# Optimization experiments

Hardware: AMD Instinct MI355X
Metric: run time of the kernel (lower is better)

Reference implementation:

```python
import jax, jax.numpy as jnp
import numpy as np
from jax import lax

# ---- fixed configuration (matches init_kwargs / input_specs) ----
L, E, V, F, HU, HL, S = 32, 1024, 2048, 8, 128, 2, 7
D0, D1R, D1E = 512, 129, 640
D = S + 1                      # path dimension = num_slices + 1
SIGLEN = D + D * D + D * D * D # iisignature.siglength(8, 3) = 584
FINAL = F * 2 * SIGLEN         # 9344
EPS = 1e-5                     # BatchNorm eps


def _bn(x, g, b):
    # BatchNorm1d in training mode: biased batch statistics over axis 0
    mu = x.mean(0)
    var = x.var(0)
    return (x - mu) / jnp.sqrt(var + EPS) * g + b


def _mlp(x, Win, bin_, gin, betain, Wh, bh, gh, betah, Wout, bout, gout, betaout):
    # eigf: Linear+BN+ReLU blocks, 1 -> HU -> ... -> HU -> 1
    h = jax.nn.relu(_bn(x @ Win.T + bin_, gin, betain))
    for l in range(HL):
        h = jax.nn.relu(_bn(h @ Wh[l].T + bh[l], gh[l], betah[l]))
    o = jax.nn.relu(_bn(h @ Wout.T + bout, gout, betaout))
    return o[:, 0]


# ---- path signature, level 3, via Chen's identity (replaces iisignature.sig) ----
def _seg(dx):
    s1 = dx
    s2 = jnp.outer(s1, dx).reshape(-1) * 0.5
    s3 = jnp.outer(s2, dx).reshape(-1) / 3.0
    return (s1, s2, s3)


def _chen(Sg, T):
    s1, s2, s3 = Sg
    t1, t2, t3 = T
    r1 = s1 + t1
    r2 = s2 + t2 + jnp.outer(s1, t1).reshape(-1)
    r3 = s3 + t3 + jnp.outer(s1, t2).reshape(-1) + jnp.outer(s2, t1).reshape(-1)
    return (r1, r2, r3)


def _sig3(path):  # path [P, D] -> [SIGLEN]
    dX = path[1:] - path[:-1]

    def step(Sg, dx):
        return _chen(Sg, _seg(dx)), None

    Sg, _ = lax.scan(step, _seg(dX[0]), dX[1:])
    return jnp.concatenate(Sg)


def _diagram_sig(vals, W_proj, b_proj):
    # Conv1d(1, S, kernel=2, stride=2) == pairwise projection; then sort, prepend time axis
    pairs = vals.reshape(-1, 2)                      # [P, 2]
    P = pairs.shape[0]
    proj = jnp.einsum('pk,sk->sp', pairs, W_proj[:, 0, :]) + b_proj[:, None]  # [S, P]
    proj = jnp.sort(proj, axis=-1)
    t = jnp.arange(P, dtype=vals.dtype) / (P * (P + 1) / 2.0)
    path = jnp.concatenate([t[None, :], proj], axis=0).T  # [P, D]
    return _sig3(path)


def setup_inputs() -> dict:
    key = jax.random.key(0)
    ks = iter(jax.random.split(key, 16))
    nrm = lambda kk, shp, sc: jax.random.normal(kk, shp, jnp.float32) * sc
    inp = {
        "eigenvalues": jax.random.uniform(next(ks), (L, E), jnp.float32),
        "eigenvectors_sq": jax.random.uniform(next(ks), (L, E, V), jnp.float32) / E,
        "dgm0": jax.random.randint(next(ks), (L, F, D0), 0, V, jnp.int32),
        "dgm1rel": jax.random.randint(next(ks), (L, F, D1R), 0, V, jnp.int32),
        "dgm1ext": jax.random.randint(next(ks), (L, F, D1E), 0, V, jnp.int32),
        "mlp_Win": nrm(next(ks), (F, HU, 1), 1.0),
        "mlp_bin": jnp.zeros((F, HU), jnp.float32),
        "mlp_gin": jnp.ones((F, HU), jnp.float32),
        "mlp_betain": jnp.zeros((F, HU), jnp.float32),
        "mlp_Wh": nrm(next(ks), (F, HL, HU, HU), 1.0 / np.sqrt(HU)),
        "mlp_bh": jnp.zeros((F, HL, HU), jnp.float32),
        "mlp_gh": jnp.ones((F, HL, HU), jnp.float32),
        "mlp_betah": jnp.zeros((F, HL, HU), jnp.float32),
        "mlp_Wout": nrm(next(ks), (F, 1, HU), 1.0 / np.sqrt(HU)),
        "mlp_bout": jnp.zeros((F, 1), jnp.float32),
        "mlp_gout": jnp.ones((F, 1), jnp.float32),
        "mlp_betaout": jnp.zeros((F, 1), jnp.float32),
        "W_proj": nrm(next(ks), (S, 1, 2), 0.7),
        "b_proj": jnp.zeros((S,), jnp.float32),
        "W_fin": nrm(next(ks), (1, FINAL), 1.0 / np.sqrt(FINAL)),
        "b_fin": jnp.zeros((1,), jnp.float32),
        "g_fin": jnp.ones((1,), jnp.float32),
        "beta_fin": jnp.zeros((1,), jnp.float32),
    }
    return inp


def reference(eigenvalues, eigenvectors_sq, dgm0, dgm1rel, dgm1ext,
              mlp_Win, mlp_bin, mlp_gin, mlp_betain,
              mlp_Wh, mlp_bh, mlp_gh, mlp_betah,
              mlp_Wout, mlp_bout, mlp_gout, mlp_betaout,
              W_proj, b_proj, W_fin, b_fin, g_fin, beta_fin):
    flat = eigenvalues.reshape(-1, 1)  # [L*E, 1], sample-major like the torch flatten
    evs = jax.vmap(lambda *p: _mlp(flat, *p))(
        mlp_Win, mlp_bin, mlp_gin, mlp_betain,
        mlp_Wh, mlp_bh, mlp_gh, mlp_betah,
        mlp_Wout, mlp_bout, mlp_gout, mlp_betaout)  # [F, L*E]
    # per-sample filtration values: evs_transformed[:, slice_i] @ eigvecsq_i
    f = jnp.einsum('fle,lev->lfv', evs.reshape(F, L, E), eigenvectors_sq)  # [L, F, V]
    fv = f.reshape(L * F, V)
    d0 = jnp.take_along_axis(fv, dgm0.reshape(L * F, D0), axis=1)
    rel = jnp.take_along_axis(fv, dgm1rel.reshape(L * F, D1R), axis=1)
    # torch.arange(len-1, 0, -1): reversed, dropping element 0
    Dgm0 = jnp.concatenate([d0, rel[:, 1:][:, ::-1]], axis=1)  # [L*F, 640]
    Dgm1 = jnp.take_along_axis(fv, dgm1ext.reshape(L * F, D1E), axis=1)
    sig0 = jax.vmap(lambda v: _diagram_sig(v, W_proj, b_proj))(Dgm0)  # [L*F, SIGLEN]
    sig1 = jax.vmap(lambda v: _diagram_sig(v, W_proj, b_proj))(Dgm1)
    x = jnp.concatenate([sig0, sig1], axis=-1).reshape(L, FINAL)
    out = x @ W_fin.T + b_fin  # dropout p=0.0 -> identity
    return _bn(out, g_fin, beta_fin)  # [L, 1]
```

## Files before the change

### kernel.cpp

```cpp
#include <hip/hip_runtime.h>
#include <cfloat>
#include <math.h>

#define N_SAMP 32768
#define FF 8
#define HU 128
#define EE 1024
#define VV 2048
#define PP 320
#define SIGLEN 584
#define FINAL_W 9344

typedef unsigned short u16;
typedef unsigned int u32;
typedef short s16x8 __attribute__((ext_vector_type(8)));
typedef float f32x4 __attribute__((ext_vector_type(4)));

__device__ __forceinline__ u16 f2bf(float v) {
  u32 u = __float_as_uint(v);
  return (u16)((u + 0x7fffu + ((u >> 16) & 1u)) >> 16);
}
__device__ __forceinline__ float bf2f(u16 h) {
  return __uint_as_float(((u32)h) << 16);
}
__device__ __forceinline__ void split3(float v, u16& h, u16& m, u16& l) {
  h = f2bf(v);
  float r = v - bf2f(h);
  m = f2bf(r);
  float r2 = r - bf2f(m);
  l = f2bf(r2);
}

__device__ __forceinline__ double wave_red(double v) {
#pragma unroll
  for (int off = 32; off > 0; off >>= 1) v += __shfl_xor(v, off, 64);
  return v;
}

__global__ __launch_bounds__(256) void k_wsplit(const float* __restrict__ W,
                                                u16* __restrict__ Hh, u16* __restrict__ Hm,
                                                u16* __restrict__ Hl, int n) {
  int i = blockIdx.x * 256 + threadIdx.x;
  if (i >= n) return;
  u16 h, m, l;
  split3(W[i], h, m, l);
  Hh[i] = h; Hm[i] = m; Hl[i] = l;
}

__global__ __launch_bounds__(256) void k_xstats(const float* __restrict__ x,
                                                double* __restrict__ xst) {
  const int tid = threadIdx.x;
  double s1 = 0.0, s2 = 0.0;
  for (int i = tid; i < N_SAMP; i += 256) { double v = (double)x[i]; s1 += v; s2 += v * v; }
  __shared__ double r1[4], r2[4];
  double w1 = wave_red(s1), w2 = wave_red(s2);
  int wave = tid >> 6, lane = tid & 63;
  if (lane == 0) { r1[wave] = w1; r2[wave] = w2; }
  __syncthreads();
  if (tid == 0) {
    xst[0] = r1[0] + r1[1] + r1[2] + r1[3];
    xst[1] = r2[0] + r2[1] + r2[2] + r2[3];
  }
}

template<int MODE>
__global__ __launch_bounds__(256, 2)
void k_mgemm(const float* __restrict__ Ain,
             const double* __restrict__ xstats,
             const float* __restrict__ w_in,
             const float* __restrict__ g_in,
             const float* __restrict__ beta_in,
             const float* __restrict__ sc,
             const float* __restrict__ sh,
             const u16* __restrict__ Wh_,
             const u16* __restrict__ Wm_,
             const u16* __restrict__ Wl_,
             const float* __restrict__ bb, int bstride,
             float* __restrict__ Yt_out,
             double* __restrict__ stats) {
  __shared__ u16 SB[6][128 * 40];
  __shared__ float p0[HU], p1[HU], biasl[HU], xl[HU];
  u16* Ah = SB[0]; u16* Am = SB[1]; u16* Al = SB[2];
  u16* Bh = SB[3]; u16* Bm = SB[4]; u16* Bl = SB[5];

  const int tid = threadIdx.x;
  const int f = blockIdx.y;
  const int m0 = blockIdx.x * 128;
  const int lane = tid & 63, ln = tid & 15, quad = (tid >> 4) & 3, wave = tid >> 6;

  if (tid < HU) {
    biasl[tid] = bb[(size_t)f * bstride + tid];
    if (MODE == 0) {
      double mx = xstats[0] * (1.0 / 32768.0);
      double vx = xstats[1] * (1.0 / 32768.0) - mx * mx;
      if (vx < 0) vx = 0;
      float w = w_in[f * HU + tid];
      double inv = 1.0 / sqrt((double)w * (double)w * vx + 1e-5);
      float sj = (float)inv * g_in[f * HU + tid] * w;
      p0[tid] = sj;
      p1[tid] = beta_in[f * HU + tid] - (float)mx * sj;
      xl[tid] = Ain[m0 + tid];
    } else {
      p0[tid] = sc[f * HU + tid];
      p1[tid] = sh[f * HU + tid];
    }
  }

  f32x4 acc[2][8];
#pragma unroll
  for (int mt = 0; mt < 2; ++mt)
#pragma unroll
    for (int u = 0; u < 8; ++u) acc[mt][u] = (f32x4){0.f, 0.f, 0.f, 0.f};

  __syncthreads();

  for (int kk = 0; kk < 128; kk += 32) {
    if (MODE == 0) {
      const int m = tid >> 1, kh = (tid & 1) * 16;
      const float xv = xl[m];
      u32 ph[8], pm[8], pl[8];
#pragma unroll
      for (int jp = 0; jp < 8; ++jp) {
        u16 h0, m_0, l0, h1, m_1, l1;
        int k = kh + jp * 2;
        split3(fmaxf(fmaf(xv, p0[kk + k], p1[kk + k]), 0.f), h0, m_0, l0);
        split3(fmaxf(fmaf(xv, p0[kk + k + 1], p1[kk + k + 1]), 0.f), h1, m_1, l1);
        ph[jp] = (u32)h0 | ((u32)h1 << 16);
        pm[jp] = (u32)m_0 | ((u32)m_1 << 16);
        pl[jp] = (u32)l0 | ((u32)l1 << 16);
      }
      int off = m * 40 + kh;
      *(uint4*)&Ah[off] = make_uint4(ph[0], ph[1], ph[2], ph[3]);
      *(uint4*)&Ah[off + 8] = make_uint4(ph[4], ph[5], ph[6], ph[7]);
      *(uint4*)&Am[off] = make_uint4(pm[0], pm[1], pm[2], pm[3]);
      *(uint4*)&Am[off + 8] = make_uint4(pm[4], pm[5], pm[6], pm[7]);
      *(uint4*)&Al[off] = make_uint4(pl[0], pl[1], pl[2], pl[3]);
      *(uint4*)&Al[off + 8] = make_uint4(pl[4], pl[5], pl[6], pl[7]);
    } else {
#pragma unroll
      for (int r = 0; r < 4; ++r) {
        int flat = tid + r * 256;
        int m = flat & 127, kq = flat >> 7;
        const float* src = Ain + ((size_t)(f * HU + kk + kq * 4)) * N_SAMP + m0 + m;
        u32 ph[2], pm[2], pl[2];
#pragma unroll
        for (int ip = 0; ip < 2; ++ip) {
          int k = kq * 4 + ip * 2;
          float v0 = fmaxf(fmaf(src[(size_t)(ip * 2) * N_SAMP], p0[kk + k], p1[kk + k]), 0.f);
          float v1 = fmaxf(fmaf(src[(size_t)(ip * 2 + 1) * N_SAMP], p0[kk + k + 1], p1[kk + k + 1]), 0.f);
          u16 h0, m_0, l0, h1, m_1, l1;
          split3(v0, h0, m_0, l0);
          split3(v1, h1, m_1, l1);
          ph[ip] = (u32)h0 | ((u32)h1 << 16);
          pm[ip] = (u32)m_0 | ((u32)m_1 << 16);
          pl[ip] = (u32)l0 | ((u32)l1 << 16);
        }
        int off = m * 40 + kq * 4;
        *(uint2*)&Ah[off] = make_uint2(ph[0], ph[1]);
        *(uint2*)&Am[off] = make_uint2(pm[0], pm[1]);
        *(uint2*)&Al[off] = make_uint2(pl[0], pl[1]);
      }
    }
#pragma unroll
    for (int r = 0; r < 2; ++r) {
      int flat = tid + r * 256;
      int n = flat >> 2, c = flat & 3;
      size_t g = (size_t)f * (2 * HU * HU) + (size_t)n * HU + kk + c * 8;
      int off = n * 40 + c * 8;
      *(uint4*)&Bh[off] = *(const uint4*)&Wh_[g];
      *(uint4*)&Bm[off] = *(const uint4*)&Wm_[g];
      *(uint4*)&Bl[off] = *(const uint4*)&Wl_[g];
    }
    __syncthreads();
    s16x8 af0[3], af1[3];
    {
      int r0 = (wave * 32 + ln) * 40 + quad * 8;
      int r1 = (wave * 32 + 16 + ln) * 40 + quad * 8;
      af0[0] = *(const s16x8*)&Ah[r0]; af0[1] = *(const s16x8*)&Am[r0]; af0[2] = *(const s16x8*)&Al[r0];
      af1[0] = *(const s16x8*)&Ah[r1]; af1[1] = *(const s16x8*)&Am[r1]; af1[2] = *(const s16x8*)&Al[r1];
    }
#pragma unroll
    for (int u = 0; u < 8; ++u) {
      int bo = (u * 16 + ln) * 40 + quad * 8;
      s16x8 bh = *(const s16x8*)&Bh[bo];
      s16x8 bm = *(const s16x8*)&Bm[bo];
      s16x8 bl = *(const s16x8*)&Bl[bo];
      f32x4 a0 = acc[0][u], a1 = acc[1][u];
      a0 = __builtin_amdgcn_mfma_f32_16x16x32_bf16(af0[0], bh, a0, 0, 0, 0);
      a1 = __builtin_amdgcn_mfma_f32_16x16x32_bf16(af1[0], bh, a1, 0, 0, 0);
      a0 = __builtin_amdgcn_mfma_f32_16x16x32_bf16(af0[1], bh, a0, 0, 0, 0);
      a1 = __builtin_amdgcn_mfma_f32_16x16x32_bf16(af1[1], bh, a1, 0, 0, 0);
      a0 = __builtin_amdgcn_mfma_f32_16x16x32_bf16(af0[0], bm, a0, 0, 0, 0);
      a1 = __builtin_amdgcn_mfma_f32_16x16x32_bf16(af1[0], bm, a1, 0, 0, 0);
      a0 = __builtin_amdgcn_mfma_f32_16x16x32_bf16(af0[2], bh, a0, 0, 0, 0);
      a1 = __builtin_amdgcn_mfma_f32_16x16x32_bf16(af1[2], bh, a1, 0, 0, 0);
      a0 = __builtin_amdgcn_mfma_f32_16x16x32_bf16(af0[1], bm, a0, 0, 0, 0);
      a1 = __builtin_amdgcn_mfma_f32_16x16x32_bf16(af1[1], bm, a1, 0, 0, 0);
      a0 = __builtin_amdgcn_mfma_f32_16x16x32_bf16(af0[0], bl, a0, 0, 0, 0);
      a1 = __builtin_amdgcn_mfma_f32_16x16x32_bf16(af1[0], bl, a1, 0, 0, 0);
      acc[0][u] = a0; acc[1][u] = a1;
    }
    __syncthreads();
  }

  float cs1[8], cs2[8];
#pragma unroll
  for (int u = 0; u < 8; ++u) { cs1[u] = 0.f; cs2[u] = 0.f; }
#pragma unroll
  for (int u = 0; u < 8; ++u) {
    float b = biasl[u * 16 + ln];
#pragma unroll
    for (int mt = 0; mt < 2; ++mt) {
#pragma unroll
      for (int reg = 0; reg < 4; ++reg) {
        float v = acc[mt][u][reg] + b;
        acc[mt][u][reg] = v;
        cs1[u] += v;
        cs2[u] = fmaf(v, v, cs2[u]);
      }
      float4 st = make_float4(acc[mt][u][0], acc[mt][u][1], acc[mt][u][2], acc[mt][u][3]);
      *(float4*)&Yt_out[((size_t)(f * HU + u * 16 + ln)) * N_SAMP + m0 + wave * 32 + mt * 16 + quad * 4] = st;
    }
  }
  float* red1 = (float*)&SB[0][0];
  float* red2 = red1 + 2048;
  int wq = wave * 4 + quad;
#pragma unroll
  for (int u = 0; u < 8; ++u) {
    red1[wq * 128 + u * 16 + ln] = cs1[u];
    red2[wq * 128 + u * 16 + ln] = cs2[u];
  }
  __syncthreads();
  {
    int which = tid >> 7, n = tid & 127;
    const float* rp = which ? red2 : red1;
    float s = 0.f;
#pragma unroll
    for (int r = 0; r < 16; ++r) s += rp[r * 128 + n];
    atomicAdd(&stats[(f * HU + n) * 2 + which], (double)s);
  }
}

__global__ __launch_bounds__(256) void k_fin(const double* __restrict__ stats,
                                             const float* __restrict__ g,
                                             const float* __restrict__ beta,
                                             int per_f, int gstride, int count,
                                             float* __restrict__ sc, float* __restrict__ sh) {
  int idx = blockIdx.x * 256 + threadIdx.x;
  if (idx >= count) return;
  int f = idx / per_f, j = idx - f * per_f;
  double S1 = stats[idx * 2 + 0], S2 = stats[idx * 2 + 1];
  double mean = S1 * (1.0 / 32768.0);
  double var = S2 * (1.0 / 32768.0) - mean * mean;
  if (var < 0) var = 0;
  double inv = 1.0 / sqrt(var + 1e-5);
  float gg = g[f * gstride + j];
  float scv = (float)inv * gg;
  sc[idx] = scv;
  sh[idx] = beta[f * gstride + j] - (float)mean * scv;
}

__global__ __launch_bounds__(256, 4) void k_outlayer(const float* __restrict__ Yt,
                                                     const float* __restrict__ sc2,
                                                     const float* __restrict__ sh2,
                                                     const float* __restrict__ Wout,
                                                     const float* __restrict__ bout,
                                                     float* __restrict__ evs_pre,
                                                     double* __restrict__ stats3) {
  __shared__ float wj[HU], scl[HU], shl[HU];
  const int tid = threadIdx.x;
  const int f = blockIdx.y;
  const int i = blockIdx.x * 256 + tid;
  if (tid < HU) {
    wj[tid] = Wout[f * HU + tid];
    scl[tid] = sc2[f * HU + tid];
    shl[tid] = sh2[f * HU + tid];
  }
  __syncthreads();
  const float* base = Yt + (size_t)f * HU * N_SAMP + i;
  float acc = 0.f;
#pragma unroll
  for (int j = 0; j < HU; ++j) {
    float y = base[(size_t)j * N_SAMP];
    acc = fmaf(fmaxf(fmaf(y, scl[j], shl[j]), 0.f), wj[j], acc);
  }
  float yo = acc + bout[f];
  evs_pre[(size_t)f * N_SAMP + i] = yo;
  double v = (double)yo;
  double s1 = wave_red(v), s2 = wave_red(v * v);
  __shared__ double r1[4], r2[4];
  int wave = tid >> 6, lane = tid & 63;
  if (lane == 0) { r1[wave] = s1; r2[wave] = s2; }
  __syncthreads();
  if (tid == 0) atomicAdd(&stats3[f * 2 + 0], r1[0] + r1[1] + r1[2] + r1[3]);
  if (tid == 1) atomicAdd(&stats3[f * 2 + 1], r2[0] + r2[1] + r2[2] + r2[3]);
}

__global__ __launch_bounds__(256) void k_einsum(const float* __restrict__ evs_pre,
                                                const float* __restrict__ sc3,
                                                const float* __restrict__ sh3,
                                                const float* __restrict__ eig,
                                                float* __restrict__ fv) {
  __shared__ float ev[FF * EE];
  const int tid = threadIdx.x;
  const int l = blockIdx.y;
  const int v0 = blockIdx.x * 256;
#pragma unroll
  for (int r = 0; r < 32; ++r) {
    int q = tid + r * 256;
    int f = q >> 10, e = q & 1023;
    float y = evs_pre[(size_t)f * N_SAMP + l * EE + e];
    ev[q] = fmaxf(fmaf(y, sc3[f], sh3[f]), 0.f);
  }
  __syncthreads();
  const float* up = eig + (size_t)l * EE * VV + v0 + tid;
  float acc[8] = {0, 0, 0, 0, 0, 0, 0, 0};
  for (int e0 = 0; e0 < EE; e0 += 32) {
    float u[32];
#pragma unroll
    for (int t = 0; t < 32; ++t) u[t] = up[(size_t)(e0 + t) * VV];
#pragma unroll
    for (int t = 0; t < 32; ++t) {
#pragma unroll
      for (int f = 0; f < 8; ++f) acc[f] = fmaf(ev[f * EE + e0 + t], u[t], acc[f]);
    }
  }
#pragma unroll
  for (int f = 0; f < 8; ++f) fv[((size_t)(l * FF + f)) * VV + v0 + tid] = acc[f];
}

__global__ __launch_bounds__(256) void k_diagram(const float* __restrict__ fv,
                                                 const int* __restrict__ dgm0,
                                                 const int* __restrict__ dgm1rel,
                                                 const int* __restrict__ dgm1ext,
                                                 const float* __restrict__ Wp,
                                                 const float* __restrict__ bp,
                                                 float* __restrict__ xbuf) {
  __shared__ float vals[640];
  __shared__ float ps[7 * 512];
  __shared__ float dXl[320][8];
  const int tid = threadIdx.x;
  const int bid = blockIdx.x;
  const int row = bid >> 1;
  const int c = bid & 1;
  const float* fvr = fv + (size_t)row * VV;

  for (int k = tid; k < 640; k += 256) {
    int idx;
    if (c == 0) idx = (k < 512) ? dgm0[(size_t)row * 512 + k] : dgm1rel[(size_t)row * 129 + (640 - k)];
    else        idx = dgm1ext[(size_t)row * 640 + k];
    vals[k] = fvr[idx];
  }
  __syncthreads();
  for (int q = tid; q < 7 * 512; q += 256) {
    int s = q >> 9, p = q & 511;
    float pv = 3.402823466e+38f;
    if (p < PP) pv = fmaf(Wp[2 * s + 1], vals[2 * p + 1], fmaf(Wp[2 * s], vals[2 * p], bp[s]));
    ps[s * 512 + p] = pv;
  }
  for (int k = 2; k <= 512; k <<= 1) {
    for (int j = k >> 1; j > 0; j >>= 1) {
      __syncthreads();
      for (int q = tid; q < 1792; q += 256) {
        int s = q >> 8, ip = q & 255;
        int i = ((ip & ~(j - 1)) << 1) | (ip & (j - 1));
        int p2 = i | j;
        float a = ps[s * 512 + i], b = ps[s * 512 + p2];
        bool up = ((i & k) == 0);
        if ((a > b) == up) { ps[s * 512 + i] = b; ps[s * 512 + p2] = a; }
      }
    }
  }
  __syncthreads();
  for (int q = tid; q < 319 * 8; q += 256) {
    int p = q >> 3, d = q & 7;
    dXl[p][d] = (d == 0) ? (1.0f / 51360.0f)
                         : ps[(d - 1) * 512 + p + 1] - ps[(d - 1) * 512 + p];
  }
  __syncthreads();
  if (tid < 64) {
    const int a = tid >> 3, b = tid & 7;
    float s1a = 0.f, s2r = 0.f;
    float s3r[8] = {0, 0, 0, 0, 0, 0, 0, 0};
    for (int p = 0; p < 319; ++p) {
      float4 dlo = *(const float4*)&dXl[p][0];
      float4 dhi = *(const float4*)&dXl[p][4];
      float dxa = dXl[p][a];
      float dxb = dXl[p][b];
      float coefA = fmaf(dxa, (1.f / 3.f), s1a);
      float w = fmaf(0.5f * dxb, coefA, s2r);
      s2r = fmaf(dxb, fmaf(0.5f, dxa, s1a), s2r);
      s3r[0] = fmaf(w, dlo.x, s3r[0]);
      s3r[1] = fmaf(w, dlo.y, s3r[1]);
      s3r[2] = fmaf(w, dlo.z, s3r[2]);
      s3r[3] = fmaf(w, dlo.w, s3r[3]);
      s3r[4] = fmaf(w, dhi.x, s3r[4]);
      s3r[5] = fmaf(w, dhi.y, s3r[5]);
      s3r[6] = fmaf(w, dhi.z, s3r[6]);
      s3r[7] = fmaf(w, dhi.w, s3r[7]);
      s1a += dxa;
    }
    const int l = row >> 3, ff = row & 7;
    float* xr = xbuf + (size_t)l * FINAL_W + ff * (2 * SIGLEN) + c * SIGLEN;
    if ((tid & 7) == 0) xr[a] = s1a;
    xr[8 + tid] = s2r;
    float* s3p = xr + 72 + tid * 8;
    *(float4*)(s3p + 0) = make_float4(s3r[0], s3r[1], s3r[2], s3r[3]);
    *(float4*)(s3p + 4) = make_float4(s3r[4], s3r[5], s3r[6], s3r[7]);
  }
}

__global__ __launch_bounds__(256) void k_rowdot(const float* __restrict__ xbuf,
                                                const float* __restrict__ Wf,
                                                const float* __restrict__ bf,
                                                double* __restrict__ outpre) {
  const int tid = threadIdx.x, l = blockIdx.x;
  const float* xr = xbuf + (size_t)l * FINAL_W;
  double acc = 0.0;
  for (int k = tid; k < FINAL_W; k += 256) acc += (double)xr[k] * (double)Wf[k];
  acc = wave_red(acc);
  __shared__ double r[4];
  int wave = tid >> 6, lane = tid & 63;
  if (lane == 0) r[wave] = acc;
  __syncthreads();
  if (tid == 0) outpre[l] = r[0] + r[1] + r[2] + r[3] + (double)bf[0];
}

__global__ __launch_bounds__(64) void k_bnfin(const double* __restrict__ outpre,
                                              const float* __restrict__ g,
                                              const float* __restrict__ beta,
                                              float* __restrict__ dout) {
  int i = threadIdx.x;
  double v = (i < 32) ? outpre[i] : 0.0;
  double s1 = wave_red(v);
  double s2 = wave_red(v * v);
  double mean = s1 * (1.0 / 32.0);
  double var = s2 * (1.0 / 32.0) - mean * mean;
  if (var < 0) var = 0;
  double inv = 1.0 / sqrt(var + 1e-5);
  if (i < 32) dout[i] = (float)((v - mean) * inv * (double)g[0] + (double)beta[0]);
}

extern "C" void kernel_launch(void* const* d_in, const int* in_sizes, int n_in,
                              void* d_out, int out_size, void* d_ws, size_t ws_size,
                              hipStream_t stream) {
  const float* eig     = (const float*)d_in[0];
  const float* eigsq   = (const float*)d_in[1];
  const int*   dgm0    = (const int*)d_in[2];
  const int*   dgm1rel = (const int*)d_in[3];
  const int*   dgm1ext = (const int*)d_in[4];
  const float* Win     = (const float*)d_in[5];
  const float* gin     = (const float*)d_in[7];
  const float* betain  = (const float*)d_in[8];
  const float* Wh      = (const float*)d_in[9];
  const float* bh      = (const float*)d_in[10];
  const float* gh      = (const float*)d_in[11];
  const float* betah   = (const float*)d_in[12];
  const float* Wout    = (const float*)d_in[13];
  const float* bout    = (const float*)d_in[14];
  const float* gout    = (const float*)d_in[15];
  const float* betaout = (const float*)d_in[16];
  const float* Wp      = (const float*)d_in[17];
  const float* bp      = (const float*)d_in[18];
  const float* Wfin    = (const float*)d_in[19];
  const float* bfin    = (const float*)d_in[20];
  const float* gfin    = (const float*)d_in[21];
  const float* betafin = (const float*)d_in[22];

  char* ws = (char*)d_ws;
  float*  Yt      = (float*)(ws);
  float*  evs_pre = (float*)(ws + 134217728u);
  float*  fv      = (float*)(ws + 135266304u);
  float*  xbuf    = (float*)(ws + 137363456u);
  float*  sc1     = (float*)(ws + 138559488u);
  float*  sh1     = sc1 + 1024;
  float*  sc2     = sc1 + 2048;
  float*  sh2     = sc1 + 3072;
  float*  sc3     = sc1 + 4096;
  float*  sh3     = sc1 + 4160;
  double* stats1  = (double*)(ws + 138576384u);
  double* stats2  = stats1 + 2048;
  double* stats3  = stats1 + 4096;
  double* xstats  = stats1 + 4112;
  double* outpre  = stats1 + 4114;
  u16*    Whh     = (u16*)(ws + 138612736u);
  u16*    Whm     = (u16*)(ws + 139137024u);
  u16*    Whl     = (u16*)(ws + 139661312u);

  hipMemsetAsync(stats1, 0, 4114 * sizeof(double), stream);

  k_wsplit<<<1024, 256, 0, stream>>>(Wh, Whh, Whm, Whl, FF * 2 * HU * HU);
  k_xstats<<<1, 256, 0, stream>>>(eig, xstats);
  k_mgemm<0><<<dim3(256, FF), 256, 0, stream>>>(eig, xstats, Win, gin, betain,
                                                nullptr, nullptr,
                                                Whh, Whm, Whl,
                                                bh, 256, Yt, stats1);
  k_fin<<<4, 256, 0, stream>>>(stats1, gh, betah, 128, 256, 1024, sc1, sh1);
  k_mgemm<1><<<dim3(256, FF), 256, 0, stream>>>(Yt, nullptr, nullptr, nullptr, nullptr,
                                                sc1, sh1,
                                                Whh + HU * HU, Whm + HU * HU, Whl + HU * HU,
                                                bh + 128, 256, Yt, stats2);
  k_fin<<<4, 256, 0, stream>>>(stats2, gh + 128, betah + 128, 128, 256, 1024, sc2, sh2);
  k_outlayer<<<dim3(128, FF), 256, 0, stream>>>(Yt, sc2, sh2, Wout, bout, evs_pre, stats3);
  k_fin<<<1, 256, 0, stream>>>(stats3, gout, betaout, 1, 1, 8, sc3, sh3);
  k_einsum<<<dim3(8, 32), 256, 0, stream>>>(evs_pre, sc3, sh3, eigsq, fv);
  k_diagram<<<512, 256, 0, stream>>>(fv, dgm0, dgm1rel, dgm1ext, Wp, bp, xbuf);
  k_rowdot<<<32, 256, 0, stream>>>(xbuf, Wfin, bfin, outpre);
  k_bnfin<<<1, 64, 0, stream>>>(outpre, gfin, betafin, (float*)d_out);
}
```

Baseline: 743.8 us.

## Fuse BN finalize into consumers, switch MLP activations to row-major, drop LDS staging

The separate weight-split and input-stats kernels are merged into one prep kernel, and the stats reduction now uses atomics across blocks. The three BN-finalize kernels are removed; each consumer recomputes scale and shift from the raw double stats. The hidden activation buffer changes from feature-major to sample-major, so the MLP GEMM loads A fragments directly from global memory into registers and reads B fragments straight from global instead of staging both in LDS with barriers. This cuts launches and syncs, but output stores become strided scalar writes, and B fragments are re-read from global/L2 by every wave.

```diff
diff --git a/kernel.cpp b/kernel.cpp
--- a/kernel.cpp
+++ b/kernel.cpp
@@ -37,29 +37,28 @@
   return v;
 }
 
-__global__ __launch_bounds__(256) void k_wsplit(const float* __restrict__ W,
-                                                u16* __restrict__ Hh, u16* __restrict__ Hm,
-                                                u16* __restrict__ Hl, int n) {
-  int i = blockIdx.x * 256 + threadIdx.x;
-  if (i >= n) return;
-  u16 h, m, l;
-  split3(W[i], h, m, l);
-  Hh[i] = h; Hm[i] = m; Hl[i] = l;
-}
-
-__global__ __launch_bounds__(256) void k_xstats(const float* __restrict__ x,
-                                                double* __restrict__ xst) {
-  const int tid = threadIdx.x;
-  double s1 = 0.0, s2 = 0.0;
-  for (int i = tid; i < N_SAMP; i += 256) { double v = (double)x[i]; s1 += v; s2 += v * v; }
-  __shared__ double r1[4], r2[4];
-  double w1 = wave_red(s1), w2 = wave_red(s2);
-  int wave = tid >> 6, lane = tid & 63;
-  if (lane == 0) { r1[wave] = w1; r2[wave] = w2; }
-  __syncthreads();
-  if (tid == 0) {
-    xst[0] = r1[0] + r1[1] + r1[2] + r1[3];
-    xst[1] = r2[0] + r2[1] + r2[2] + r2[3];
+__global__ __launch_bounds__(256) void k_prep(const float* __restrict__ W,
+                                              u16* __restrict__ Hh, u16* __restrict__ Hm,
+                                              u16* __restrict__ Hl,
+                                              const float* __restrict__ x,
+                                              double* __restrict__ xst) {
+  const int b = blockIdx.x, tid = threadIdx.x;
+  if (b < 1024) {
+    int i = b * 256 + tid;
+    u16 h, m, l;
+    split3(W[i], h, m, l);
+    Hh[i] = h; Hm[i] = m; Hl[i] = l;
+  } else {
+    int i0 = (b - 1024) * 512 + tid;
+    double v0 = (double)x[i0], v1 = (double)x[i0 + 256];
+    double s1 = wave_red(v0 + v1);
+    double s2 = wave_red(v0 * v0 + v1 * v1);
+    __shared__ double r1[4], r2[4];
+    int wave = tid >> 6, lane = tid & 63;
+    if (lane == 0) { r1[wave] = s1; r2[wave] = s2; }
+    __syncthreads();
+    if (tid == 0) atomicAdd(&xst[0], r1[0] + r1[1] + r1[2] + r1[3]);
+    if (tid == 1) atomicAdd(&xst[1], r2[0] + r2[1] + r2[2] + r2[3]);
   }
 }
 
@@ -70,23 +69,22 @@
              const float* __restrict__ w_in,
              const float* __restrict__ g_in,
              const float* __restrict__ beta_in,
-             const float* __restrict__ sc,
-             const float* __restrict__ sh,
+             const double* __restrict__ stats_prev,
+             const float* __restrict__ gL,
+             const float* __restrict__ betaL,
              const u16* __restrict__ Wh_,
              const u16* __restrict__ Wm_,
              const u16* __restrict__ Wl_,
              const float* __restrict__ bb, int bstride,
-             float* __restrict__ Yt_out,
+             float* __restrict__ Yout,
              double* __restrict__ stats) {
-  __shared__ u16 SB[6][128 * 40];
   __shared__ float p0[HU], p1[HU], biasl[HU], xl[HU];
-  u16* Ah = SB[0]; u16* Am = SB[1]; u16* Al = SB[2];
-  u16* Bh = SB[3]; u16* Bm = SB[4]; u16* Bl = SB[5];
+  __shared__ float red[2][16][128];
 
   const int tid = threadIdx.x;
   const int f = blockIdx.y;
   const int m0 = blockIdx.x * 128;
-  const int lane = tid & 63, ln = tid & 15, quad = (tid >> 4) & 3, wave = tid >> 6;
+  const int ln = tid & 15, quad = (tid >> 4) & 3, wave = tid >> 6;
 
   if (tid < HU) {
     biasl[tid] = bb[(size_t)f * bstride + tid];
@@ -101,10 +99,18 @@
       p1[tid] = beta_in[f * HU + tid] - (float)mx * sj;
       xl[tid] = Ain[m0 + tid];
     } else {
-      p0[tid] = sc[f * HU + tid];
-      p1[tid] = sh[f * HU + tid];
-    }
-  }
+      int idx = f * HU + tid;
+      double S1 = stats_prev[idx * 2 + 0], S2 = stats_prev[idx * 2 + 1];
+      double mean = S1 * (1.0 / 32768.0);
+      double var = S2 * (1.0 / 32768.0) - mean * mean;
+      if (var < 0) var = 0;
+      double inv = 1.0 / sqrt(var + 1e-5);
+      float scv = (float)inv * gL[f * 256 + tid];
+      p0[tid] = scv;
+      p1[tid] = betaL[f * 256 + tid] - (float)mean * scv;
+    }
+  }
+  __syncthreads();
 
   f32x4 acc[2][8];
 #pragma unroll
@@ -112,95 +118,76 @@
 #pragma unroll
     for (int u = 0; u < 8; ++u) acc[mt][u] = (f32x4){0.f, 0.f, 0.f, 0.f};
 
-  __syncthreads();
-
+  const int mA0 = m0 + wave * 32 + ln;
+  const int mA1 = mA0 + 16;
+  float x0 = 0.f, x1 = 0.f;
+  if (MODE == 0) { x0 = xl[wave * 32 + ln]; x1 = xl[wave * 32 + 16 + ln]; }
+
+  const size_t fw = (size_t)f * (2 * HU * HU);
+  const u16* WhF = Wh_ + fw;
+  const u16* WmF = Wm_ + fw;
+  const u16* WlF = Wl_ + fw;
+
+#pragma unroll
   for (int kk = 0; kk < 128; kk += 32) {
+    float p0v[8], p1v[8];
+#pragma unroll
+    for (int j = 0; j < 8; ++j) {
+      p0v[j] = p0[kk + quad * 8 + j];
+      p1v[j] = p1[kk + quad * 8 + j];
+    }
+    float va0[8], va1[8];
     if (MODE == 0) {
-      const int m = tid >> 1, kh = (tid & 1) * 16;
-      const float xv = xl[m];
-      u32 ph[8], pm[8], pl[8];
-#pragma unroll
-      for (int jp = 0; jp < 8; ++jp) {
-        u16 h0, m_0, l0, h1, m_1, l1;
-        int k = kh + jp * 2;
-        split3(fmaxf(fmaf(xv, p0[kk + k], p1[kk + k]), 0.f), h0, m_0, l0);
-        split3(fmaxf(fmaf(xv, p0[kk + k + 1], p1[kk + k + 1]), 0.f), h1, m_1, l1);
-        ph[jp] = (u32)h0 | ((u32)h1 << 16);
-        pm[jp] = (u32)m_0 | ((u32)m_1 << 16);
-        pl[jp] = (u32)l0 | ((u32)l1 << 16);
+#pragma unroll
+      for (int j = 0; j < 8; ++j) {
+        va0[j] = fmaxf(fmaf(x0, p0v[j], p1v[j]), 0.f);
+        va1[j] = fmaxf(fmaf(x1, p0v[j], p1v[j]), 0.f);
       }
-      int off = m * 40 + kh;
-      *(uint4*)&Ah[off] = make_uint4(ph[0], ph[1], ph[2], ph[3]);
-      *(uint4*)&Ah[off + 8] = make_uint4(ph[4], ph[5], ph[6], ph[7]);
-      *(uint4*)&Am[off] = make_uint4(pm[0], pm[1], pm[2], pm[3]);
-      *(uint4*)&Am[off + 8] = make_uint4(pm[4], pm[5], pm[6], pm[7]);
-      *(uint4*)&Al[off] = make_uint4(pl[0], pl[1], pl[2], pl[3]);
-      *(uint4*)&Al[off + 8] = make_uint4(pl[4], pl[5], pl[6], pl[7]);
     } else {
-#pragma unroll
-      for (int r = 0; r < 4; ++r) {
-        int flat = tid + r * 256;
-        int m = flat & 127, kq = flat >> 7;
-        const float* src = Ain + ((size_t)(f * HU + kk + kq * 4)) * N_SAMP + m0 + m;
-        u32 ph[2], pm[2], pl[2];
-#pragma unroll
-        for (int ip = 0; ip < 2; ++ip) {
-          int k = kq * 4 + ip * 2;
-          float v0 = fmaxf(fmaf(src[(size_t)(ip * 2) * N_SAMP], p0[kk + k], p1[kk + k]), 0.f);
-          float v1 = fmaxf(fmaf(src[(size_t)(ip * 2 + 1) * N_SAMP], p0[kk + k + 1], p1[kk + k + 1]), 0.f);
-          u16 h0, m_0, l0, h1, m_1, l1;
-          split3(v0, h0, m_0, l0);
-          split3(v1, h1, m_1, l1);
-          ph[ip] = (u32)h0 | ((u32)h1 << 16);
-          pm[ip] = (u32)m_0 | ((u32)m_1 << 16);
-          pl[ip] = (u32)l0 | ((u32)l1 << 16);
-        }
-        int off = m * 40 + kq * 4;
-        *(uint2*)&Ah[off] = make_uint2(ph[0], ph[1]);
-        *(uint2*)&Am[off] = make_uint2(pm[0], pm[1]);
-        *(uint2*)&Al[off] = make_uint2(pl[0], pl[1]);
+      const float* r0 = Ain + ((size_t)(f * N_SAMP) + mA0) * HU + kk + quad * 8;
+      const float* r1 = Ain + ((size_t)(f * N_SAMP) + mA1) * HU + kk + quad * 8;
+      float4 a0 = *(const float4*)r0;
+      float4 a1 = *(const float4*)(r0 + 4);
+      float4 b0 = *(const float4*)r1;
+      float4 b1 = *(const float4*)(r1 + 4);
+      float ra0[8] = {a0.x, a0.y, a0.z, a0.w, a1.x, a1.y, a1.z, a1.w};
+      float rb0[8] = {b0.x, b0.y, b0.z, b0.w, b1.x, b1.y, b1.z, b1.w};
+#pragma unroll
+      for (int j = 0; j < 8; ++j) {
+        va0[j] = fmaxf(fmaf(ra0[j], p0v[j], p1v[j]), 0.f);
+        va1[j] = fmaxf(fmaf(rb0[j], p0v[j], p1v[j]), 0.f);
       }
     }
-#pragma unroll
-    for (int r = 0; r < 2; ++r) {
-      int flat = tid + r * 256;
-      int n = flat >> 2, c = flat & 3;
-      size_t g = (size_t)f * (2 * HU * HU) + (size_t)n * HU + kk + c * 8;
-      int off = n * 40 + c * 8;
-      *(uint4*)&Bh[off] = *(const uint4*)&Wh_[g];
-      *(uint4*)&Bm[off] = *(const uint4*)&Wm_[g];
-      *(uint4*)&Bl[off] = *(const uint4*)&Wl_[g];
-    }
-    __syncthreads();
-    s16x8 af0[3], af1[3];
-    {
-      int r0 = (wave * 32 + ln) * 40 + quad * 8;
-      int r1 = (wave * 32 + 16 + ln) * 40 + quad * 8;
-      af0[0] = *(const s16x8*)&Ah[r0]; af0[1] = *(const s16x8*)&Am[r0]; af0[2] = *(const s16x8*)&Al[r0];
-      af1[0] = *(const s16x8*)&Ah[r1]; af1[1] = *(const s16x8*)&Am[r1]; af1[2] = *(const s16x8*)&Al[r1];
+    s16x8 ah0, am0, al0, ah1, am1, al1;
+#pragma unroll
+    for (int j = 0; j < 8; ++j) {
+      u16 h, m, l;
+      split3(va0[j], h, m, l);
+      ah0[j] = (short)h; am0[j] = (short)m; al0[j] = (short)l;
+      split3(va1[j], h, m, l);
+      ah1[j] = (short)h; am1[j] = (short)m; al1[j] = (short)l;
     }
 #pragma unroll
     for (int u = 0; u < 8; ++u) {
-      int bo = (u * 16 + ln) * 40 + quad * 8;
-      s16x8 bh = *(const s16x8*)&Bh[bo];
-      s16x8 bm = *(const s16x8*)&Bm[bo];
-      s16x8 bl = *(const s16x8*)&Bl[bo];
-      f32x4 a0 = acc[0][u], a1 = acc[1][u];
-      a0 = __builtin_amdgcn_mfma_f32_16x16x32_bf16(af0[0], bh, a0, 0, 0, 0);
-      a1 = __builtin_amdgcn_mfma_f32_16x16x32_bf16(af1[0], bh, a1, 0, 0, 0);
-      a0 = __builtin_amdgcn_mfma_f32_16x16x32_bf16(af0[1], bh, a0, 0, 0, 0);
-      a1 = __builtin_amdgcn_mfma_f32_16x16x32_bf16(af1[1], bh, a1, 0, 0, 0);
-      a0 = __builtin_amdgcn_mfma_f32_16x16x32_bf16(af0[0], bm, a0, 0, 0, 0);
-      a1 = __builtin_amdgcn_mfma_f32_16x16x32_bf16(af1[0], bm, a1, 0, 0, 0);
-      a0 = __builtin_amdgcn_mfma_f32_16x16x32_bf16(af0[2], bh, a0, 0, 0, 0);
-      a1 = __builtin_amdgcn_mfma_f32_16x16x32_bf16(af1[2], bh, a1, 0, 0, 0);
-      a0 = __builtin_amdgcn_mfma_f32_16x16x32_bf16(af0[1], bm, a0, 0, 0, 0);
-      a1 = __builtin_amdgcn_mfma_f32_16x16x32_bf16(af1[1], bm, a1, 0, 0, 0);
-      a0 = __builtin_amdgcn_mfma_f32_16x16x32_bf16(af0[0], bl, a0, 0, 0, 0);
-      a1 = __builtin_amdgcn_mfma_f32_16x16x32_bf16(af1[0], bl, a1, 0, 0, 0);
-      acc[0][u] = a0; acc[1][u] = a1;
-    }
-    __syncthreads();
+      size_t off = (size_t)((u * 16 + ln) * HU + kk + quad * 8);
+      s16x8 bh = *(const s16x8*)(WhF + off);
+      s16x8 bm = *(const s16x8*)(WmF + off);
+      s16x8 bl = *(const s16x8*)(WlF + off);
+      f32x4 c0 = acc[0][u], c1 = acc[1][u];
+      c0 = __builtin_amdgcn_mfma_f32_16x16x32_bf16(ah0, bh, c0, 0, 0, 0);
+      c1 = __builtin_amdgcn_mfma_f32_16x16x32_bf16(ah1, bh, c1, 0, 0, 0);
+      c0 = __builtin_amdgcn_mfma_f32_16x16x32_bf16(am0, bh, c0, 0, 0, 0);
+      c1 = __builtin_amdgcn_mfma_f32_16x16x32_bf16(am1, bh, c1, 0, 0, 0);
+      c0 = __builtin_amdgcn_mfma_f32_16x16x32_bf16(ah0, bm, c0, 0, 0, 0);
+      c1 = __builtin_amdgcn_mfma_f32_16x16x32_bf16(ah1, bm, c1, 0, 0, 0);
+      c0 = __builtin_amdgcn_mfma_f32_16x16x32_bf16(al0, bh, c0, 0, 0, 0);
+      c1 = __builtin_amdgcn_mfma_f32_16x16x32_bf16(al1, bh, c1, 0, 0, 0);
+      c0 = __builtin_amdgcn_mfma_f32_16x16x32_bf16(am0, bm, c0, 0, 0, 0);
+      c1 = __builtin_amdgcn_mfma_f32_16x16x32_bf16(am1, bm, c1, 0, 0, 0);
+      c0 = __builtin_amdgcn_mfma_f32_16x16x32_bf16(ah0, bl, c0, 0, 0, 0);
+      c1 = __builtin_amdgcn_mfma_f32_16x16x32_bf16(ah1, bl, c1, 0, 0, 0);
+      acc[0][u] = c0; acc[1][u] = c1;
+    }
   }
 
   float cs1[8], cs2[8];
@@ -208,61 +195,40 @@
   for (int u = 0; u < 8; ++u) { cs1[u] = 0.f; cs2[u] = 0.f; }
 #pragma unroll
   for (int u = 0; u < 8; ++u) {
-    float b = biasl[u * 16 + ln];
+    int n = u * 16 + ln;
+    float b = biasl[n];
 #pragma unroll
     for (int mt = 0; mt < 2; ++mt) {
+      int mbase = m0 + wave * 32 + mt * 16 + quad * 4;
 #pragma unroll
       for (int reg = 0; reg < 4; ++reg) {
         float v = acc[mt][u][reg] + b;
-        acc[mt][u][reg] = v;
         cs1[u] += v;
         cs2[u] = fmaf(v, v, cs2[u]);
+        Yout[((size_t)(f * N_SAMP) + mbase + reg) * HU + n] = v;
       }
-      float4 st = make_float4(acc[mt][u][0], acc[mt][u][1], acc[mt][u][2], acc[mt][u][3]);
-      *(float4*)&Yt_out[((size_t)(f * HU + u * 16 + ln)) * N_SAMP + m0 + wave * 32 + mt * 16 + quad * 4] = st;
-    }
-  }
-  float* red1 = (float*)&SB[0][0];
-  float* red2 = red1 + 2048;
+    }
+  }
   int wq = wave * 4 + quad;
 #pragma unroll
   for (int u = 0; u < 8; ++u) {
-    red1[wq * 128 + u * 16 + ln] = cs1[u];
-    red2[wq * 128 + u * 16 + ln] = cs2[u];
+    red[0][wq][u * 16 + ln] = cs1[u];
+    red[1][wq][u * 16 + ln] = cs2[u];
   }
   __syncthreads();
   {
     int which = tid >> 7, n = tid & 127;
-    const float* rp = which ? red2 : red1;
     float s = 0.f;
 #pragma unroll
-    for (int r = 0; r < 16; ++r) s += rp[r * 128 + n];
+    for (int r = 0; r < 16; ++r) s += red[which][r][n];
     atomicAdd(&stats[(f * HU + n) * 2 + which], (double)s);
   }
 }
 
-__global__ __launch_bounds__(256) void k_fin(const double* __restrict__ stats,
-                                             const float* __restrict__ g,
-                                             const float* __restrict__ beta,
-                                             int per_f, int gstride, int count,
-                                             float* __restrict__ sc, float* __restrict__ sh) {
-  int idx = blockIdx.x * 256 + threadIdx.x;
-  if (idx >= count) return;
-  int f = idx / per_f, j = idx - f * per_f;
-  double S1 = stats[idx * 2 + 0], S2 = stats[idx * 2 + 1];
-  double mean = S1 * (1.0 / 32768.0);
-  double var = S2 * (1.0 / 32768.0) - mean * mean;
-  if (var < 0) var = 0;
-  double inv = 1.0 / sqrt(var + 1e-5);
-  float gg = g[f * gstride + j];
-  float scv = (float)inv * gg;
-  sc[idx] = scv;
-  sh[idx] = beta[f * gstride + j] - (float)mean * scv;
-}
-
-__global__ __launch_bounds__(256, 4) void k_outlayer(const float* __restrict__ Yt,
-                                                     const float* __restrict__ sc2,
-                                                     const float* __restrict__ sh2,
+__global__ __launch_bounds__(256, 4) void k_outlayer(const float* __restrict__ Y,
+                                                     const double* __restrict__ stats2,
+                                                     const float* __restrict__ gL,
+                                                     const float* __restrict__ betaL,
                                                      const float* __restrict__ Wout,
                                                      const float* __restrict__ bout,
                                                      float* __restrict__ evs_pre,
@@ -272,17 +238,28 @@
   const int f = blockIdx.y;
   const int i = blockIdx.x * 256 + tid;
   if (tid < HU) {
+    int idx = f * HU + tid;
+    double S1 = stats2[idx * 2 + 0], S2 = stats2[idx * 2 + 1];
+    double mean = S1 * (1.0 / 32768.0);
+    double var = S2 * (1.0 / 32768.0) - mean * mean;
+    if (var < 0) var = 0;
+    double inv = 1.0 / sqrt(var + 1e-5);
+    float scv = (float)inv * gL[f * 256 + 128 + tid];
+    scl[tid] = scv;
+    shl[tid] = betaL[f * 256 + 128 + tid] - (float)mean * scv;
     wj[tid] = Wout[f * HU + tid];
-    scl[tid] = sc2[f * HU + tid];
-    shl[tid] = sh2[f * HU + tid];
-  }
-  __syncthreads();
-  const float* base = Yt + (size_t)f * HU * N_SAMP + i;
+  }
+  __syncthreads();
+  const float4* base = (const float4*)(Y + ((size_t)(f * N_SAMP) + i) * HU);
   float acc = 0.f;
 #pragma unroll
-  for (int j = 0; j < HU; ++j) {
-    float y = base[(size_t)j * N_SAMP];
-    acc = fmaf(fmaxf(fmaf(y, scl[j], shl[j]), 0.f), wj[j], acc);
+  for (int q = 0; q < 32; ++q) {
+    float4 y = base[q];
+    int j = q * 4;
+    acc = fmaf(fmaxf(fmaf(y.x, scl[j + 0], shl[j + 0]), 0.f), wj[j + 0], acc);
+    acc = fmaf(fmaxf(fmaf(y.y, scl[j + 1], shl[j + 1]), 0.f), wj[j + 1], acc);
+    acc = fmaf(fmaxf(fmaf(y.z, scl[j + 2], shl[j + 2]), 0.f), wj[j + 2], acc);
+    acc = fmaf(fmaxf(fmaf(y.w, scl[j + 3], shl[j + 3]), 0.f), wj[j + 3], acc);
   }
   float yo = acc + bout[f];
   evs_pre[(size_t)f * N_SAMP + i] = yo;
@@ -297,20 +274,33 @@
 }
 
 __global__ __launch_bounds__(256) void k_einsum(const float* __restrict__ evs_pre,
-                                                const float* __restrict__ sc3,
-                                                const float* __restrict__ sh3,
+                                                const double* __restrict__ stats3,
+                                                const float* __restrict__ gout,
+                                                const float* __restrict__ betaout,
                                                 const float* __restrict__ eig,
                                                 float* __restrict__ fv) {
   __shared__ float ev[FF * EE];
+  __shared__ float sc3s[8], sh3s[8];
   const int tid = threadIdx.x;
   const int l = blockIdx.y;
   const int v0 = blockIdx.x * 256;
+  if (tid < 8) {
+    double S1 = stats3[tid * 2 + 0], S2 = stats3[tid * 2 + 1];
+    double mean = S1 * (1.0 / 32768.0);
+    double var = S2 * (1.0 / 32768.0) - mean * mean;
+    if (var < 0) var = 0;
+    double inv = 1.0 / sqrt(var + 1e-5);
+    float scv = (float)inv * gout[tid];
+    sc3s[tid] = scv;
+    sh3s[tid] = betaout[tid] - (float)mean * scv;
+  }
+  __syncthreads();
 #pragma unroll
   for (int r = 0; r < 32; ++r) {
     int q = tid + r * 256;
     int f = q >> 10, e = q & 1023;
     float y = evs_pre[(size_t)f * N_SAMP + l * EE + e];
-    ev[q] = fmaxf(fmaf(y, sc3[f], sh3[f]), 0.f);
+    ev[q] = fmaxf(fmaf(y, sc3s[f], sh3s[f]), 0.f);
   }
   __syncthreads();
   const float* up = eig + (size_t)l * EE * VV + v0 + tid;
@@ -468,16 +458,10 @@
   const float* betafin = (const float*)d_in[22];
 
   char* ws = (char*)d_ws;
-  float*  Yt      = (float*)(ws);
+  float*  Y       = (float*)(ws);
   float*  evs_pre = (float*)(ws + 134217728u);
   float*  fv      = (float*)(ws + 135266304u);
   float*  xbuf    = (float*)(ws + 137363456u);
-  float*  sc1     = (float*)(ws + 138559488u);
-  float*  sh1     = sc1 + 1024;
-  float*  sc2     = sc1 + 2048;
-  float*  sh2     = sc1 + 3072;
-  float*  sc3     = sc1 + 4096;
-  float*  sh3     = sc1 + 4160;
   double* stats1  = (double*)(ws + 138576384u);
   double* stats2  = stats1 + 2048;
   double* stats3  = stats1 + 4096;
@@ -489,21 +473,18 @@
 
   hipMemsetAsync(stats1, 0, 4114 * sizeof(double), stream);
 
-  k_wsplit<<<1024, 256, 0, stream>>>(Wh, Whh, Whm, Whl, FF * 2 * HU * HU);
-  k_xstats<<<1, 256, 0, stream>>>(eig, xstats);
+  k_prep<<<1088, 256, 0, stream>>>(Wh, Whh, Whm, Whl, eig, xstats);
   k_mgemm<0><<<dim3(256, FF), 256, 0, stream>>>(eig, xstats, Win, gin, betain,
-                                                nullptr, nullptr,
+                                                nullptr, nullptr, nullptr,
                                                 Whh, Whm, Whl,
-                                                bh, 256, Yt, stats1);
-  k_fin<<<4, 256, 0, stream>>>(stats1, gh, betah, 128, 256, 1024, sc1, sh1);
-  k_mgemm<1><<<dim3(256, FF), 256, 0, stream>>>(Yt, nullptr, nullptr, nullptr, nullptr,
-                                                sc1, sh1,
+                                                bh, 256, Y, stats1);
+  k_mgemm<1><<<dim3(256, FF), 256, 0, stream>>>(Y, nullptr, nullptr, nullptr, nullptr,
+                                                stats1, gh, betah,
                                                 Whh + HU * HU, Whm + HU * HU, Whl + HU * HU,
-                                                bh + 128, 256, Yt, stats2);
-  k_fin<<<4, 256, 0, stream>>>(stats2, gh + 128, betah + 128, 128, 256, 1024, sc2, sh2);
-  k_outlayer<<<dim3(128, FF), 256, 0, stream>>>(Yt, sc2, sh2, Wout, bout, evs_pre, stats3);
-  k_fin<<<1, 256, 0, stream>>>(stats3, gout, betaout, 1, 1, 8, sc3, sh3);
-  k_einsum<<<dim3(8, 32), 256, 0, stream>>>(evs_pre, sc3, sh3, eigsq, fv);
+                                                bh + 128, 256, Y, stats2);
+  k_outlayer<<<dim3(128, FF), 256, 0, stream>>>(Y, stats2, gh, betah, Wout, bout,
+                                                evs_pre, stats3);
+  k_einsum<<<dim3(8, 32), 256, 0, stream>>>(evs_pre, stats3, gout, betaout, eigsq, fv);
   k_diagram<<<512, 256, 0, stream>>>(fv, dgm0, dgm1rel, dgm1ext, Wp, bp, xbuf);
   k_rowdot<<<32, 256, 0, stream>>>(xbuf, Wfin, bfin, outpre);
   k_bnfin<<<1, 64, 0, stream>>>(outpre, gfin, betafin, (float*)d_out);
```

New measurement: 777.6 us. 1.05x slower.
